# Kernel optimization log

Measured on AMD Instinct MI355X. Metric: run time of the kernel, lower is better.

The kernel has to match this reference:

```python
import jax, jax.numpy as jnp
import numpy as np
import math

B, MSA, L, D = 1, 64, 256, 512
H = 8
DH = D // H  # 64


def setup_inputs() -> dict:
    key = jax.random.key(0)
    ks = jax.random.split(key, 6)
    x = jax.random.normal(ks[0], (B, MSA, L, D), dtype=jnp.float32)
    Wq = jax.random.normal(ks[1], (D, D), dtype=jnp.float32) * (1.0 / math.sqrt(D))
    Wk = jax.random.normal(ks[2], (D, D), dtype=jnp.float32) * (1.0 / math.sqrt(D))
    Wv = jax.random.normal(ks[3], (D, D), dtype=jnp.float32) * (1.0 / math.sqrt(D))
    aK = jax.random.normal(ks[4], (L, L, DH), dtype=jnp.float32)
    aV = jax.random.normal(ks[5], (L, L, DH), dtype=jnp.float32)
    return {"x": x, "Wq": Wq, "Wk": Wk, "Wv": Wv, "aK": aK, "aV": aV}


def _proj(t, W, b, m, l, h, dh):
    # nn.Linear(bias=False): t @ W.T, then split heads -> (B,H,MSA,L,dh)
    y = jnp.einsum('bmld,ed->bmle', t, W).reshape(b, m, l, h, dh)
    return jnp.transpose(y, (0, 3, 1, 2, 4))


def reference(x, Wq, Wk, Wv, aK, aV):
    b, m, l, d = x.shape
    h, dh = H, DH
    q = _proj(x, Wq, b, m, l, h, dh)  # (B,H,MSA,L,dh)
    k = _proj(x, Wk, b, m, l, h, dh)
    v = _proj(x, Wv, b, m, l, h, dh)
    # content score + relative-position score
    e1 = jnp.einsum('bhmid,bhmjd->bhmij', q, k)           # (B,H,MSA,L,L)
    e2 = jnp.einsum('bhmid,ijd->bhmij', q, aK)            # (B,H,MSA,L,L)
    alpha = jax.nn.softmax((e1 + e2) / math.sqrt(dh), axis=-1)
    z1 = jnp.einsum('bhmij,bhmjd->bhmid', alpha, v)       # content output
    z2 = jnp.einsum('bhmij,ijd->bhmid', alpha, aV)        # relative-V output
    z = (z1 + z2).sum(axis=2)                             # sum over MSA -> (B,H,L,dh)
    out = jnp.transpose(z, (0, 2, 1, 3)).reshape(b, l, d) # (B,L,D)
    return out
```

## Files before the change

### kernel.cpp

```cpp
#include <hip/hip_runtime.h>

#define THREADS 256

typedef unsigned short u16;
typedef __attribute__((ext_vector_type(8))) short bf16x8;
typedef __attribute__((ext_vector_type(4))) float f32x4;

__device__ __forceinline__ u16 f2bf(float f) {
  unsigned int u = __float_as_uint(f);
  u += 0x7fffu + ((u >> 16) & 1u);
  return (u16)(u >> 16);
}
__device__ __forceinline__ float bf2f(u16 s) {
  return __uint_as_float(((unsigned int)s) << 16);
}
__device__ __forceinline__ bf16x8 ld8g(const u16* p) {
  return *reinterpret_cast<const bf16x8*>(p);
}
__device__ __forceinline__ bf16x8 ld8s(const u16* p) {
  return *reinterpret_cast<const bf16x8*>(p);
}
__device__ __forceinline__ void st4bf(u16* dst, float4 v) {
  unsigned int lo = (unsigned int)f2bf(v.x) | ((unsigned int)f2bf(v.y) << 16);
  unsigned int hi = (unsigned int)f2bf(v.z) | ((unsigned int)f2bf(v.w) << 16);
  uint2 u; u.x = lo; u.y = hi;
  *reinterpret_cast<uint2*>(dst) = u;
}
__device__ __forceinline__ uint4 pack8(float4 a, float4 b) {
  uint4 r;
  r.x = (unsigned int)f2bf(a.x) | ((unsigned int)f2bf(a.y) << 16);
  r.y = (unsigned int)f2bf(a.z) | ((unsigned int)f2bf(a.w) << 16);
  r.z = (unsigned int)f2bf(b.x) | ((unsigned int)f2bf(b.y) << 16);
  r.w = (unsigned int)f2bf(b.z) | ((unsigned int)f2bf(b.w) << 16);
  return r;
}
typedef __attribute__((address_space(1))) const unsigned int g_u32;
typedef __attribute__((address_space(3))) unsigned int l_u32;
__device__ __forceinline__ void async16(const u16* g, u16* l) {
  __builtin_amdgcn_global_load_lds((g_u32*)g, (l_u32*)l, 16, 0, 0);
}

__global__ __launch_bounds__(THREADS) void cast_xw(
    const float* __restrict__ x, const float* __restrict__ wq,
    const float* __restrict__ wk, const float* __restrict__ wv,
    u16* __restrict__ xb, u16* __restrict__ wqb, u16* __restrict__ wkb,
    u16* __restrict__ wvb) {
  int t = blockIdx.x * THREADS + threadIdx.x;
  if (t < 2097152) {
    st4bf(xb + t * 4, reinterpret_cast<const float4*>(x)[t]);
  } else if (t < 2162688) {
    int q = t - 2097152;
    st4bf(wqb + q * 4, reinterpret_cast<const float4*>(wq)[q]);
  } else if (t < 2228224) {
    int q = t - 2162688;
    st4bf(wkb + q * 4, reinterpret_cast<const float4*>(wk)[q]);
  } else if (t < 2293760) {
    int q = t - 2228224;
    st4bf(wvb + q * 4, reinterpret_cast<const float4*>(wv)[q]);
  }
}

__global__ __launch_bounds__(THREADS) void proj_gemm(
    const u16* __restrict__ xb, const u16* __restrict__ wb,
    u16* __restrict__ qh, u16* __restrict__ kb, u16* __restrict__ vt) {
  const int bm = blockIdx.x / 12, bn = blockIdx.x % 12;
  const int tid = threadIdx.x;
  const int wave = tid >> 6, lane = tid & 63;
  const int quad = lane >> 4, l15 = lane & 15;
  __shared__ __align__(16) u16 smem[9216];
  u16* At = smem;
  u16* Bt = smem + 4096;

  const int rowL = lane >> 2;
  const int chunkL = (lane & 3) ^ ((lane >> 3) & 3);
  const u16* gA = xb + (size_t)(bm * 128 + wave * 32 + rowL) * 512 + chunkL * 8;
  const u16* gB = wb + (size_t)(bn * 128 + wave * 32 + rowL) * 512 + chunkL * 8;
  u16* lA = At + wave * 1024;
  u16* lB = Bt + wave * 1024;

  const int rw0 = (wave & 1) * 64, cw0 = (wave >> 1) * 64;
  const int swz = (quad ^ ((l15 >> 1) & 3)) * 8;

  f32x4 acc[4][4];
#pragma unroll
  for (int mt = 0; mt < 4; ++mt)
#pragma unroll
    for (int nt = 0; nt < 4; ++nt) acc[mt][nt] = (f32x4){0.f, 0.f, 0.f, 0.f};

  for (int s = 0; s < 16; ++s) {
    __syncthreads();
    async16(gA + s * 32, lA);
    async16(gA + s * 32 + 8192, lA + 512);
    async16(gB + s * 32, lB);
    async16(gB + s * 32 + 8192, lB + 512);
    __syncthreads();
    bf16x8 af[4], bf[4];
#pragma unroll
    for (int mt = 0; mt < 4; ++mt)
      af[mt] = ld8s(At + (rw0 + mt * 16 + l15) * 32 + swz);
#pragma unroll
    for (int nt = 0; nt < 4; ++nt)
      bf[nt] = ld8s(Bt + (cw0 + nt * 16 + l15) * 32 + swz);
#pragma unroll
    for (int mt = 0; mt < 4; ++mt)
#pragma unroll
      for (int nt = 0; nt < 4; ++nt)
        acc[mt][nt] = __builtin_amdgcn_mfma_f32_16x16x32_bf16(af[mt], bf[nt], acc[mt][nt], 0, 0, 0);
  }

  const int mat = bn >> 2;
  const int h0 = (bn & 3) * 2;
  const int m = bm >> 1;
  const int l0 = (bm & 1) * 128;

  if (mat < 2) {
    u16* dstb = (mat == 0) ? qh : kb;
    const int il = tid >> 1, cc = (tid & 1) * 32;
#pragma unroll
    for (int p = 0; p < 2; ++p) {
      __syncthreads();
      if ((wave >> 1) == p) {
#pragma unroll
        for (int mt = 0; mt < 4; ++mt)
#pragma unroll
          for (int nt = 0; nt < 4; ++nt)
#pragma unroll
            for (int r = 0; r < 4; ++r)
              smem[(rw0 + mt * 16 + quad * 4 + r) * 72 + nt * 16 + l15] =
                  f2bf(acc[mt][nt][r]);
      }
      __syncthreads();
      u16* dst = dstb + ((size_t)((h0 + p) * 64 + m) * 256 + l0 + il) * 64 + cc;
      uint4 v0 = *reinterpret_cast<uint4*>(&smem[il * 72 + cc]);
      uint4 v1 = *reinterpret_cast<uint4*>(&smem[il * 72 + cc + 8]);
      uint4 v2 = *reinterpret_cast<uint4*>(&smem[il * 72 + cc + 16]);
      uint4 v3 = *reinterpret_cast<uint4*>(&smem[il * 72 + cc + 24]);
      *reinterpret_cast<uint4*>(dst) = v0;
      *reinterpret_cast<uint4*>(dst + 8) = v1;
      *reinterpret_cast<uint4*>(dst + 16) = v2;
      *reinterpret_cast<uint4*>(dst + 24) = v3;
    }
  } else {
    const int tl = tid >> 2, cc = (tid & 3) * 32;
#pragma unroll
    for (int p = 0; p < 2; ++p) {
      __syncthreads();
      if ((wave >> 1) == p) {
#pragma unroll
        for (int mt = 0; mt < 4; ++mt)
#pragma unroll
          for (int nt = 0; nt < 4; ++nt)
#pragma unroll
            for (int r = 0; r < 4; ++r)
              smem[(nt * 16 + l15) * 136 + rw0 + mt * 16 + quad * 4 + r] =
                  f2bf(acc[mt][nt][r]);
      }
      __syncthreads();
      int hm = (h0 + p) * 64 + m;
      u16* dst = vt + (size_t)hm * 16384 + tl * 256 + l0 + cc;
      uint4 v0 = *reinterpret_cast<uint4*>(&smem[tl * 136 + cc]);
      uint4 v1 = *reinterpret_cast<uint4*>(&smem[tl * 136 + cc + 8]);
      uint4 v2 = *reinterpret_cast<uint4*>(&smem[tl * 136 + cc + 16]);
      uint4 v3 = *reinterpret_cast<uint4*>(&smem[tl * 136 + cc + 24]);
      *reinterpret_cast<uint4*>(dst) = v0;
      *reinterpret_cast<uint4*>(dst + 8) = v1;
      *reinterpret_cast<uint4*>(dst + 16) = v2;
      *reinterpret_cast<uint4*>(dst + 24) = v3;
    }
  }
}

__global__ __launch_bounds__(THREADS) void e2_k(
    const u16* __restrict__ qh, const float* __restrict__ aK,
    u16* __restrict__ e2g) {
  const int i = blockIdx.x >> 3, hmt = blockIdx.x & 7;
  const int tid = threadIdx.x;
  const int wave = tid >> 6, lane = tid & 63;
  const int quad = lane >> 4, l15 = lane & 15;
  __shared__ u16 aKl[256 * 72];
#pragma unroll
  for (int c = 0; c < 8; ++c) {
    int fidx = c * 2048 + tid * 8;
    int j = fidx >> 6, d = fidx & 63;
    float4 f0 = *reinterpret_cast<const float4*>(aK + i * 16384 + fidx);
    float4 f1 = *reinterpret_cast<const float4*>(aK + i * 16384 + fidx + 4);
    *reinterpret_cast<uint4*>(&aKl[j * 72 + d]) = pack8(f0, f1);
  }
  __syncthreads();
  f32x4 acc[16];
#pragma unroll
  for (int nt = 0; nt < 16; ++nt) acc[nt] = (f32x4){0.f, 0.f, 0.f, 0.f};
  bf16x8 a[2];
#pragma unroll
  for (int ks = 0; ks < 2; ++ks)
    a[ks] = ld8g(qh + ((hmt * 64 + wave * 16 + l15) * 256 + i) * 64 + ks * 32 + quad * 8);
#pragma unroll
  for (int nt = 0; nt < 16; ++nt) {
#pragma unroll
    for (int ks = 0; ks < 2; ++ks) {
      bf16x8 b = ld8s(&aKl[(nt * 16 + l15) * 72 + ks * 32 + quad * 8]);
      acc[nt] = __builtin_amdgcn_mfma_f32_16x16x32_bf16(a[ks], b, acc[nt], 0, 0, 0);
    }
  }
  __syncthreads();
  u16* S = aKl;
#pragma unroll
  for (int nt = 0; nt < 16; ++nt)
#pragma unroll
    for (int r = 0; r < 4; ++r)
      S[(wave * 16 + quad * 4 + r) * 264 + nt * 16 + l15] = f2bf(acc[nt][r]);
  __syncthreads();
#pragma unroll
  for (int c = 0; c < 8; ++c) {
    int lin = c * 2048 + tid * 8;
    int row = lin >> 8, col = lin & 255;
    uint4 v = *reinterpret_cast<uint4*>(&S[row * 264 + col]);
    *reinterpret_cast<uint4*>(e2g + ((size_t)(hmt * 64 + row) * 256 + i) * 256 + col) = v;
  }
}

__global__ __launch_bounds__(THREADS, 2) void attn_f(
    const u16* __restrict__ qh, const u16* __restrict__ kb,
    const u16* __restrict__ vt, const u16* __restrict__ e2g,
    u16* __restrict__ betap, u16* __restrict__ z1q) {
  const int bi = blockIdx.x;
  const int it = bi >> 7;
  const int hmc = bi & 127;
  const int h = hmc >> 4, mc = hmc & 15;
  const int tid = threadIdx.x;
  const int wave = tid >> 6, lane = tid & 63;
  const int quad = lane >> 4, l15 = lane & 15;
  __shared__ u16 As[4 * 4224];
  u16* W = &As[wave * 4224];
  const int i0 = it * 64 + wave * 16;

  f32x4 betaacc[16];
  f32x4 acc2[4];
#pragma unroll
  for (int nt = 0; nt < 16; ++nt) betaacc[nt] = (f32x4){0.f, 0.f, 0.f, 0.f};
#pragma unroll
  for (int nt = 0; nt < 4; ++nt) acc2[nt] = (f32x4){0.f, 0.f, 0.f, 0.f};

  for (int mi = 0; mi < 4; ++mi) {
    const int hm = h * 64 + mc * 4 + mi;
    f32x4 acc[16];
    const u16* e2p = e2g + ((size_t)hm * 256 + i0 + quad * 4) * 256 + l15;
#pragma unroll
    for (int nt = 0; nt < 16; ++nt)
#pragma unroll
      for (int r = 0; r < 4; ++r)
        acc[nt][r] = bf2f(e2p[r * 256 + nt * 16]);
    bf16x8 a[2];
#pragma unroll
    for (int ks = 0; ks < 2; ++ks)
      a[ks] = ld8g(qh + ((size_t)hm * 256 + i0 + l15) * 64 + ks * 32 + quad * 8);
#pragma unroll
    for (int nt = 0; nt < 16; ++nt) {
#pragma unroll
      for (int ks = 0; ks < 2; ++ks) {
        bf16x8 b = ld8g(kb + ((size_t)hm * 256 + nt * 16 + l15) * 64 + ks * 32 + quad * 8);
        acc[nt] = __builtin_amdgcn_mfma_f32_16x16x32_bf16(a[ks], b, acc[nt], 0, 0, 0);
      }
    }
#pragma unroll
    for (int r = 0; r < 4; ++r) {
      float mx = -3.0e38f;
#pragma unroll
      for (int nt = 0; nt < 16; ++nt) mx = fmaxf(mx, acc[nt][r]);
      for (int msk = 1; msk < 16; msk <<= 1) mx = fmaxf(mx, __shfl_xor(mx, msk));
      float s = 0.f;
#pragma unroll
      for (int nt = 0; nt < 16; ++nt) {
        float p = expf((acc[nt][r] - mx) * 0.125f);
        acc[nt][r] = p;
        s += p;
      }
      for (int msk = 1; msk < 16; msk <<= 1) s += __shfl_xor(s, msk);
      float inv = 1.0f / s;
      int lrow = quad * 4 + r;
#pragma unroll
      for (int nt = 0; nt < 16; ++nt) {
        float av = acc[nt][r] * inv;
        betaacc[nt][r] += av;
        W[lrow * 264 + nt * 16 + l15] = f2bf(av);
      }
    }
#pragma unroll
    for (int ks = 0; ks < 8; ++ks) {
      bf16x8 a2 = ld8s(&W[l15 * 264 + ks * 32 + quad * 8]);
#pragma unroll
      for (int nt = 0; nt < 4; ++nt) {
        bf16x8 b2 = ld8g(vt + (size_t)hm * 16384 + (nt * 16 + l15) * 256 + ks * 32 + quad * 8);
        acc2[nt] = __builtin_amdgcn_mfma_f32_16x16x32_bf16(a2, b2, acc2[nt], 0, 0, 0);
      }
    }
  }

#pragma unroll
  for (int nt = 0; nt < 16; ++nt)
#pragma unroll
    for (int r = 0; r < 4; ++r)
      W[(quad * 4 + r) * 264 + nt * 16 + l15] = f2bf(betaacc[nt][r]);
#pragma unroll
  for (int c = 0; c < 8; ++c) {
    int lin = c * 512 + lane * 8;
    int row = lin >> 8, col = lin & 255;
    uint4 v = *reinterpret_cast<uint4*>(&W[row * 264 + col]);
    *reinterpret_cast<uint4*>(
        betap + ((size_t)hmc * 256 + it * 64 + wave * 16 + row) * 256 + col) = v;
  }
#pragma unroll
  for (int nt = 0; nt < 4; ++nt)
#pragma unroll
    for (int r = 0; r < 4; ++r)
      W[(quad * 4 + r) * 72 + nt * 16 + l15] = f2bf(acc2[nt][r]);
  {
    int row = lane >> 2, col = (lane & 3) * 16;
    uint4 v0 = *reinterpret_cast<uint4*>(&W[row * 72 + col]);
    uint4 v1 = *reinterpret_cast<uint4*>(&W[row * 72 + col + 8]);
    u16* dst = z1q + ((size_t)hmc * 256 + it * 64 + wave * 16 + row) * 64 + col;
    *reinterpret_cast<uint4*>(dst) = v0;
    *reinterpret_cast<uint4*>(dst + 8) = v1;
  }
}

__global__ __launch_bounds__(THREADS) void beta_r(
    const u16* __restrict__ betap, float* __restrict__ beta) {
  int t = blockIdx.x * THREADS + threadIdx.x;
  int hi = t >> 5;
  int j0 = (t & 31) * 8;
  int h = hi >> 8, i = hi & 255;
  const u16* src = betap + ((size_t)(h * 16) * 256 + i) * 256 + j0;
  float s[8] = {0.f, 0.f, 0.f, 0.f, 0.f, 0.f, 0.f, 0.f};
#pragma unroll
  for (int m = 0; m < 16; ++m) {
    uint4 v = *reinterpret_cast<const uint4*>(src + (size_t)m * 65536);
    const u16* pv = reinterpret_cast<const u16*>(&v);
#pragma unroll
    for (int u = 0; u < 8; ++u) s[u] += bf2f(pv[u]);
  }
  float4 o0 = {s[0], s[1], s[2], s[3]};
  float4 o1 = {s[4], s[5], s[6], s[7]};
  *reinterpret_cast<float4*>(beta + (size_t)hi * 256 + j0) = o0;
  *reinterpret_cast<float4*>(beta + (size_t)hi * 256 + j0 + 4) = o1;
}

__global__ __launch_bounds__(THREADS) void z2_k(
    const float* __restrict__ beta, const float* __restrict__ aV,
    float* __restrict__ z2b) {
  const int i = blockIdx.x;
  const int tid = threadIdx.x;
  const int wave = tid >> 6, lane = tid & 63;
  const int quad = lane >> 4, l15 = lane & 15;
  __shared__ u16 aVl[64 * 264];
#pragma unroll
  for (int c = 0; c < 8; ++c) {
    int fidx = c * 2048 + tid * 8;
    int j = fidx >> 6, d = fidx & 63;
    float4 f0 = *reinterpret_cast<const float4*>(aV + (size_t)i * 16384 + fidx);
    float4 f1 = *reinterpret_cast<const float4*>(aV + (size_t)i * 16384 + fidx + 4);
    float fv[8] = {f0.x, f0.y, f0.z, f0.w, f1.x, f1.y, f1.z, f1.w};
#pragma unroll
    for (int u = 0; u < 8; ++u) aVl[(d + u) * 264 + j] = f2bf(fv[u]);
  }
  __syncthreads();
  f32x4 acc = (f32x4){0.f, 0.f, 0.f, 0.f};
#pragma unroll
  for (int ks = 0; ks < 8; ++ks) {
    u16 ab[8];
    if (l15 < 8) {
      const float* bp = beta + (l15 * 256 + i) * 256 + ks * 32 + quad * 8;
      float4 f0 = *reinterpret_cast<const float4*>(bp);
      float4 f1 = *reinterpret_cast<const float4*>(bp + 4);
      ab[0] = f2bf(f0.x); ab[1] = f2bf(f0.y); ab[2] = f2bf(f0.z); ab[3] = f2bf(f0.w);
      ab[4] = f2bf(f1.x); ab[5] = f2bf(f1.y); ab[6] = f2bf(f1.z); ab[7] = f2bf(f1.w);
    } else {
#pragma unroll
      for (int u = 0; u < 8; ++u) ab[u] = 0;
    }
    bf16x8 a = *reinterpret_cast<bf16x8*>(ab);
    bf16x8 b = ld8s(&aVl[(wave * 16 + l15) * 264 + ks * 32 + quad * 8]);
    acc = __builtin_amdgcn_mfma_f32_16x16x32_bf16(a, b, acc, 0, 0, 0);
  }
#pragma unroll
  for (int r = 0; r < 4; ++r) {
    int hh = quad * 4 + r;
    if (hh < 8) z2b[i * 512 + hh * 64 + wave * 16 + l15] = acc[r];
  }
}

__global__ __launch_bounds__(THREADS) void final_k(
    const u16* __restrict__ z1q, const float* __restrict__ z2b,
    float* __restrict__ out) {
  int o = blockIdx.x * THREADS + threadIdx.x;
  int i = o >> 9, e = o & 511;
  int h = e >> 6, d = e & 63;
  float s = z2b[o];
  const u16* base = z1q + ((size_t)(h * 16) * 256 + i) * 64 + d;
#pragma unroll
  for (int m = 0; m < 16; ++m) s += bf2f(base[(size_t)m * 16384]);
  out[o] = s;
}

extern "C" void kernel_launch(void* const* d_in, const int* in_sizes, int n_in,
                              void* d_out, int out_size, void* d_ws, size_t ws_size,
                              hipStream_t stream) {
  const float* x  = (const float*)d_in[0];
  const float* wq = (const float*)d_in[1];
  const float* wk = (const float*)d_in[2];
  const float* wv = (const float*)d_in[3];
  const float* aK = (const float*)d_in[4];
  const float* aV = (const float*)d_in[5];
  float* out = (float*)d_out;

  char* ws = (char*)d_ws;
  u16* xb    = (u16*)(ws + 0);
  u16* wqb   = (u16*)(ws + 16777216);
  u16* wkb   = (u16*)(ws + 17301504);
  u16* wvb   = (u16*)(ws + 17825792);
  u16* betap = (u16*)(ws + 18350080);
  u16* qh    = (u16*)(ws + 35127296);
  u16* kb    = (u16*)(ws + 51904512);
  u16* vt    = (u16*)(ws + 68681728);
  u16* e2g   = (u16*)(ws + 85458944);
  u16* z1q   = xb;
  float* beta= (float*)(ws + 4194304);
  float* z2b = (float*)(ws + 6291456);

  cast_xw<<<8960, THREADS, 0, stream>>>(x, wq, wk, wv, xb, wqb, wkb, wvb);
  proj_gemm<<<1536, THREADS, 0, stream>>>(xb, wqb, qh, kb, vt);
  e2_k<<<2048, THREADS, 0, stream>>>(qh, aK, e2g);
  attn_f<<<512, THREADS, 0, stream>>>(qh, kb, vt, e2g, betap, z1q);
  beta_r<<<256, THREADS, 0, stream>>>(betap, beta);
  z2_k<<<256, THREADS, 0, stream>>>(beta, aV, z2b);
  final_k<<<512, THREADS, 0, stream>>>(z1q, z2b, out);
}
```

Baseline: 283.5 us.

## Fuse beta reduction, z2 and final sum; swizzle GEMM blocks; stage q in LDS

```diff
diff --git a/kernel.cpp b/kernel.cpp
--- a/kernel.cpp
+++ b/kernel.cpp
@@ -63,7 +63,9 @@
 __global__ __launch_bounds__(THREADS) void proj_gemm(
     const u16* __restrict__ xb, const u16* __restrict__ wb,
     u16* __restrict__ qh, u16* __restrict__ kb, u16* __restrict__ vt) {
-  const int bm = blockIdx.x / 12, bn = blockIdx.x % 12;
+  const int bid = blockIdx.x;
+  const int swzb = (bid & 7) * 192 + (bid >> 3);
+  const int bm = swzb / 12, bn = swzb % 12;
   const int tid = threadIdx.x;
   const int wave = tid >> 6, lane = tid & 63;
   const int quad = lane >> 4, l15 = lane & 15;
@@ -173,11 +175,12 @@
 __global__ __launch_bounds__(THREADS) void e2_k(
     const u16* __restrict__ qh, const float* __restrict__ aK,
     u16* __restrict__ e2g) {
-  const int i = blockIdx.x >> 3, hmt = blockIdx.x & 7;
+  const int hmt = blockIdx.x >> 8, i = blockIdx.x & 255;
   const int tid = threadIdx.x;
   const int wave = tid >> 6, lane = tid & 63;
   const int quad = lane >> 4, l15 = lane & 15;
   __shared__ u16 aKl[256 * 72];
+  __shared__ u16 qL[64 * 72];
 #pragma unroll
   for (int c = 0; c < 8; ++c) {
     int fidx = c * 2048 + tid * 8;
@@ -186,6 +189,14 @@
     float4 f1 = *reinterpret_cast<const float4*>(aK + i * 16384 + fidx + 4);
     *reinterpret_cast<uint4*>(&aKl[j * 72 + d]) = pack8(f0, f1);
   }
+#pragma unroll
+  for (int c = 0; c < 4; ++c) {
+    int r = c * 16 + (tid >> 4);
+    int dd = (tid & 15) * 4;
+    uint2 v = *reinterpret_cast<const uint2*>(
+        qh + ((size_t)(hmt * 64 + r) * 256 + i) * 64 + dd);
+    *reinterpret_cast<uint2*>(&qL[r * 72 + dd]) = v;
+  }
   __syncthreads();
   f32x4 acc[16];
 #pragma unroll
@@ -193,7 +204,7 @@
   bf16x8 a[2];
 #pragma unroll
   for (int ks = 0; ks < 2; ++ks)
-    a[ks] = ld8g(qh + ((hmt * 64 + wave * 16 + l15) * 256 + i) * 64 + ks * 32 + quad * 8);
+    a[ks] = ld8s(&qL[(wave * 16 + l15) * 72 + ks * 32 + quad * 8]);
 #pragma unroll
   for (int nt = 0; nt < 16; ++nt) {
 #pragma unroll
@@ -271,7 +282,7 @@
       float s = 0.f;
 #pragma unroll
       for (int nt = 0; nt < 16; ++nt) {
-        float p = expf((acc[nt][r] - mx) * 0.125f);
+        float p = __expf((acc[nt][r] - mx) * 0.125f);
         acc[nt][r] = p;
         s += p;
       }
@@ -324,35 +335,16 @@
   }
 }
 
-__global__ __launch_bounds__(THREADS) void beta_r(
-    const u16* __restrict__ betap, float* __restrict__ beta) {
-  int t = blockIdx.x * THREADS + threadIdx.x;
-  int hi = t >> 5;
-  int j0 = (t & 31) * 8;
-  int h = hi >> 8, i = hi & 255;
-  const u16* src = betap + ((size_t)(h * 16) * 256 + i) * 256 + j0;
-  float s[8] = {0.f, 0.f, 0.f, 0.f, 0.f, 0.f, 0.f, 0.f};
-#pragma unroll
-  for (int m = 0; m < 16; ++m) {
-    uint4 v = *reinterpret_cast<const uint4*>(src + (size_t)m * 65536);
-    const u16* pv = reinterpret_cast<const u16*>(&v);
-#pragma unroll
-    for (int u = 0; u < 8; ++u) s[u] += bf2f(pv[u]);
-  }
-  float4 o0 = {s[0], s[1], s[2], s[3]};
-  float4 o1 = {s[4], s[5], s[6], s[7]};
-  *reinterpret_cast<float4*>(beta + (size_t)hi * 256 + j0) = o0;
-  *reinterpret_cast<float4*>(beta + (size_t)hi * 256 + j0 + 4) = o1;
-}
-
-__global__ __launch_bounds__(THREADS) void z2_k(
-    const float* __restrict__ beta, const float* __restrict__ aV,
-    float* __restrict__ z2b) {
+__global__ __launch_bounds__(THREADS) void z2f_k(
+    const u16* __restrict__ betap, const u16* __restrict__ z1q,
+    const float* __restrict__ aV, float* __restrict__ out) {
   const int i = blockIdx.x;
   const int tid = threadIdx.x;
   const int wave = tid >> 6, lane = tid & 63;
   const int quad = lane >> 4, l15 = lane & 15;
   __shared__ u16 aVl[64 * 264];
+  __shared__ float bj[8 * 256];
+  __shared__ float z2L[512];
 #pragma unroll
   for (int c = 0; c < 8; ++c) {
     int fidx = c * 2048 + tid * 8;
@@ -363,17 +355,29 @@
 #pragma unroll
     for (int u = 0; u < 8; ++u) aVl[(d + u) * 264 + j] = f2bf(fv[u]);
   }
+  {
+    int h = tid >> 5, j0 = (tid & 31) * 8;
+    const u16* src = betap + (size_t)(h * 16) * 65536 + i * 256 + j0;
+    float s[8] = {0.f, 0.f, 0.f, 0.f, 0.f, 0.f, 0.f, 0.f};
+#pragma unroll
+    for (int m = 0; m < 16; ++m) {
+      uint4 v = *reinterpret_cast<const uint4*>(src + (size_t)m * 65536);
+      const u16* pv = reinterpret_cast<const u16*>(&v);
+#pragma unroll
+      for (int u = 0; u < 8; ++u) s[u] += bf2f(pv[u]);
+    }
+#pragma unroll
+    for (int u = 0; u < 8; ++u) bj[h * 256 + j0 + u] = s[u];
+  }
   __syncthreads();
   f32x4 acc = (f32x4){0.f, 0.f, 0.f, 0.f};
 #pragma unroll
   for (int ks = 0; ks < 8; ++ks) {
     u16 ab[8];
     if (l15 < 8) {
-      const float* bp = beta + (l15 * 256 + i) * 256 + ks * 32 + quad * 8;
-      float4 f0 = *reinterpret_cast<const float4*>(bp);
-      float4 f1 = *reinterpret_cast<const float4*>(bp + 4);
-      ab[0] = f2bf(f0.x); ab[1] = f2bf(f0.y); ab[2] = f2bf(f0.z); ab[3] = f2bf(f0.w);
-      ab[4] = f2bf(f1.x); ab[5] = f2bf(f1.y); ab[6] = f2bf(f1.z); ab[7] = f2bf(f1.w);
+      const float* bp = &bj[l15 * 256 + ks * 32 + quad * 8];
+#pragma unroll
+      for (int u = 0; u < 8; ++u) ab[u] = f2bf(bp[u]);
     } else {
 #pragma unroll
       for (int u = 0; u < 8; ++u) ab[u] = 0;
@@ -385,21 +389,19 @@
 #pragma unroll
   for (int r = 0; r < 4; ++r) {
     int hh = quad * 4 + r;
-    if (hh < 8) z2b[i * 512 + hh * 64 + wave * 16 + l15] = acc[r];
-  }
-}
-
-__global__ __launch_bounds__(THREADS) void final_k(
-    const u16* __restrict__ z1q, const float* __restrict__ z2b,
-    float* __restrict__ out) {
-  int o = blockIdx.x * THREADS + threadIdx.x;
-  int i = o >> 9, e = o & 511;
-  int h = e >> 6, d = e & 63;
-  float s = z2b[o];
-  const u16* base = z1q + ((size_t)(h * 16) * 256 + i) * 64 + d;
-#pragma unroll
-  for (int m = 0; m < 16; ++m) s += bf2f(base[(size_t)m * 16384]);
-  out[o] = s;
+    if (hh < 8) z2L[hh * 64 + wave * 16 + l15] = acc[r];
+  }
+  __syncthreads();
+#pragma unroll
+  for (int c = 0; c < 2; ++c) {
+    int e = c * 256 + tid;
+    int h = e >> 6, d = e & 63;
+    float s = z2L[e];
+    const u16* base = z1q + ((size_t)(h * 16) * 256 + i) * 64 + d;
+#pragma unroll
+    for (int m = 0; m < 16; ++m) s += bf2f(base[(size_t)m * 16384]);
+    out[(size_t)i * 512 + e] = s;
+  }
 }
 
 extern "C" void kernel_launch(void* const* d_in, const int* in_sizes, int n_in,
@@ -424,14 +426,10 @@
   u16* vt    = (u16*)(ws + 68681728);
   u16* e2g   = (u16*)(ws + 85458944);
   u16* z1q   = xb;
-  float* beta= (float*)(ws + 4194304);
-  float* z2b = (float*)(ws + 6291456);
 
   cast_xw<<<8960, THREADS, 0, stream>>>(x, wq, wk, wv, xb, wqb, wkb, wvb);
   proj_gemm<<<1536, THREADS, 0, stream>>>(xb, wqb, qh, kb, vt);
   e2_k<<<2048, THREADS, 0, stream>>>(qh, aK, e2g);
   attn_f<<<512, THREADS, 0, stream>>>(qh, kb, vt, e2g, betap, z1q);
-  beta_r<<<256, THREADS, 0, stream>>>(betap, beta);
-  z2_k<<<256, THREADS, 0, stream>>>(beta, aV, z2b);
-  final_k<<<512, THREADS, 0, stream>>>(z1q, z2b, out);
-}
+  z2f_k<<<256, THREADS, 0, stream>>>(betap, z1q, aV, out);
+}
```

Measured after the change: 261.3 us. -7.8%, faster.
